# Kernel optimization log

Measured on AMD Instinct MI355X. Metric: run time of the kernel, lower is better.

Reference implementation:

```python
import jax, jax.numpy as jnp
import numpy as np

# DynamicMaskHead config (CondLaneHead defaults, head_layers=3, channels=64)
N, INS_PER_IMG, C, H, W = 4, 8, 64, 160, 256
CIN = C + 2  # coords concatenated
L1, L2, L3 = (C + 2) * C, C * C, C * 1  # weight_nums = [4224, 4096, 64]
B1, B2, B3 = C, C, 1                     # bias_nums   = [64, 64, 1]
NUM_PARAMS = L1 + L2 + L3 + B1 + B2 + B3  # 8513
MASK_BIAS_SHIFT = 2.19  # subtracted from last bias when is_mask=True


def setup_inputs() -> dict:
    key = jax.random.key(0)
    k1, k2 = jax.random.split(key)
    x = jax.random.normal(k1, (N, C, H, W), dtype=jnp.float32)
    mask_head_params = jax.random.normal(k2, (N * INS_PER_IMG, NUM_PARAMS), dtype=jnp.float32) * 0.05
    num_ins = np.full((N,), INS_PER_IMG, dtype=np.int32)  # static per-image instance counts
    return {"x": x, "mask_head_params": mask_head_params, "num_ins": num_ins}


def _locations(h, w, dtype):
    # compute_locations with stride=1: +stride//2 == +0; original normalization
    # (locations[:0], locations[:1]) is a no-op slice, so coords stay unnormalized.
    loc_x = jnp.broadcast_to(jnp.arange(w, dtype=dtype)[None, :], (h, w))
    loc_y = jnp.broadcast_to(jnp.arange(h, dtype=dtype)[:, None], (h, w))
    return jnp.stack([loc_x, loc_y], axis=0)  # [2, H, W]


def reference(x, mask_head_params, num_ins):
    n, _, h, w = x.shape
    loc = _locations(h, w, x.dtype)
    xa = jnp.concatenate([jnp.broadcast_to(loc[None], (n, 2, h, w)), x], axis=1)  # [N, 66, H, W]

    # replicate each image's features per instance (grouped-conv input)
    img_idx = np.repeat(np.arange(n), np.asarray(num_ins))  # static
    num_insts = img_idx.shape[0]
    feats = xa[img_idx].reshape(num_insts, CIN, h * w)  # [I, 66, L]

    # parse_dynamic_params: split flat params into per-instance 1x1 conv weights/biases
    splits = jnp.split(mask_head_params, np.cumsum([L1, L2, L3, B1, B2]), axis=1)
    w0 = splits[0].reshape(num_insts, C, CIN)
    w1 = splits[1].reshape(num_insts, C, C)
    w2 = splits[2].reshape(num_insts, 1, C)
    b0 = splits[3]
    b1 = splits[4]
    b2 = splits[5] - MASK_BIAS_SHIFT  # is_mask=True

    # grouped 1x1 convs == per-instance small matmuls (batched GEMM)
    hdn = jax.nn.relu(jnp.einsum('ioc,icl->iol', w0, feats) + b0[:, :, None])
    hdn = jax.nn.relu(jnp.einsum('ioc,icl->iol', w1, hdn) + b1[:, :, None])
    out = jnp.einsum('ioc,icl->iol', w2, hdn) + b2[:, :, None]  # [I, 1, L]
    return out.reshape(1, num_insts, h, w)
```

## Files before the change

kernel.cpp:

```cpp
#include <hip/hip_runtime.h>
#include <hip/hip_bf16.h>


#define NP 8513
#define HW 40960
#define ISTRIDE 18432
#define OFF_VECA 8192
#define OFF_W1 9216
#define OFF_VECB 17408

typedef __attribute__((ext_vector_type(8))) short bf16x8;
typedef __attribute__((ext_vector_type(4))) float f32x4;
typedef __attribute__((ext_vector_type(2))) unsigned uint2v;

__device__ inline unsigned short f2bf(float f) {
  union { float f; unsigned u; } v; v.f = f;
  unsigned r = v.u + 0x7fffu + ((v.u >> 16) & 1u);
  return (unsigned short)(r >> 16);
}
__device__ inline unsigned pk2(float a, float b) {
  __hip_bfloat162 h = __float22bfloat162_rn(float2{a, b});
  union { __hip_bfloat162 h; unsigned u; } v; v.h = h;
  return v.u;
}
__device__ inline void gld16(const void* g, void* l) {
  __builtin_amdgcn_global_load_lds(
      (const __attribute__((address_space(1))) unsigned*)g,
      (__attribute__((address_space(3))) unsigned*)l, 16, 0, 0);
}

__global__ void condlane_prep(const float* __restrict__ params,
                              char* __restrict__ ws) {
  const int inst = blockIdx.x >> 3, part = blockIdx.x & 7;
  const float* __restrict__ p = params + inst * NP;
  char* base = ws + inst * ISTRIDE;
  const int t = threadIdx.x;
  if (part < 4) {
    unsigned short* dst = (unsigned short*)base;
#pragma unroll
    for (int it = 0; it < 4; it++) {
      const int e = (part * 4 + it) * 256 + t;
      const int frag = e >> 9, lane = (e >> 3) & 63, j = e & 7;
      const int m = (frag >> 1) * 16 + (lane & 15);
      const int k = (frag & 1) * 32 + ((lane >> 4) << 3) + j;
      dst[e] = f2bf(p[m * 66 + 2 + k]);
    }
  } else {
    unsigned short* dst = (unsigned short*)(base + OFF_W1);
#pragma unroll
    for (int it = 0; it < 4; it++) {
      const int e = ((part - 4) * 4 + it) * 256 + t;
      const int frag = e >> 9, lane = (e >> 3) & 63, j = e & 7;
      const int m = (frag >> 1) * 16 + (lane & 15);
      const int k = (frag & 1) * 32 + ((lane >> 4) << 3) + j;
      dst[e] = f2bf(p[4224 + m * 64 + k]);
    }
    if (part == 4) {
      float* vA = (float*)(base + OFF_VECA);
      float* vB = (float*)(base + OFF_VECB);
      if (t < 64) {
        vA[t]       = p[8384 + t];
        vA[64 + t]  = p[t * 66];
        vA[128 + t] = p[t * 66 + 1];
        vB[t]       = p[8448 + t];
        vB[64 + t]  = p[8320 + t];
      } else if (t == 64) vB[128] = p[8512] - 2.19f;
    }
  }
}

__global__ __launch_bounds__(256, 4) void condlane_main(
    const float* __restrict__ x, const char* __restrict__ ws,
    float* __restrict__ out) {
  __shared__ __align__(16) char smem[2 * ISTRIDE];
  const int img = blockIdx.y, bx = blockIdx.x;
  const int tid = threadIdx.x, lane = tid & 63, wave = tid >> 6;
  const int col = lane & 15, q = lane >> 4;
  const char* const wsb = ws + img * 8 * ISTRIDE;

  auto dma = [&](int i, char* buf) {
    const char* src = wsb + i * ISTRIDE;
#pragma unroll
    for (int u = 0; u < 4; u++) {
      const int off = (wave * 4 + u) * 1024;
      gld16(src + off + lane * 16, buf + off);
    }
    if (wave < 2) {
      const int off = (16 + wave) * 1024;
      gld16(src + off + lane * 16, buf + off);
    }
  };
  dma(0, smem);

  bf16x8 bfr[2];
  {
    const float* gx = x + img * 64 * HW + bx * 64 + wave * 16;
#pragma unroll
    for (int ks = 0; ks < 2; ks++) {
      float f[8];
#pragma unroll
      for (int j = 0; j < 8; j++)
        f[j] = gx[(ks * 32 + q * 8 + j) * HW + col];
      union { bf16x8 v; unsigned d[4]; } u;
#pragma unroll
      for (int jj = 0; jj < 4; jj++) u.d[jj] = pk2(f[2 * jj], f[2 * jj + 1]);
      bfr[ks] = u.v;
    }
  }
  __syncthreads();

  const float fyv = (float)(bx >> 2);
  const float fxv = (float)((bx & 3) * 64 + wave * 16 + col);
  float* const outb = out + img * 8 * HW + bx * 64 + wave * 16;

  for (int i = 0; i < 8; i++) {
    char* const wb = smem + (i & 1) * ISTRIDE;
    if (i < 7) dma(i + 1, smem + ((i + 1) & 1) * ISTRIDE);
    const float* const vecA = (const float*)(wb + OFF_VECA);
    const float* const vecB = (const float*)(wb + OFF_VECB);

    f32x4 acc[4];
#pragma unroll
    for (int mt = 0; mt < 4; mt++) {
      const int ro = mt * 16 + q * 4;
      const f32x4 b0v = *(const f32x4*)(vecA + ro);
      const f32x4 wxv = *(const f32x4*)(vecA + 64 + ro);
      const f32x4 wyv = *(const f32x4*)(vecA + 128 + ro);
      acc[mt] = (b0v + wyv * fyv) + wxv * fxv;
    }
#pragma unroll
    for (int mt = 0; mt < 4; mt++) {
      const bf16x8 a0 = *(const bf16x8*)(wb + (mt * 2 + 0) * 1024 + lane * 16);
      const bf16x8 a1 = *(const bf16x8*)(wb + (mt * 2 + 1) * 1024 + lane * 16);
      f32x4 c = __builtin_amdgcn_mfma_f32_16x16x32_bf16(a0, bfr[0], acc[mt], 0, 0, 0);
      acc[mt] = __builtin_amdgcn_mfma_f32_16x16x32_bf16(a1, bfr[1], c, 0, 0, 0);
    }

    unsigned pd[4][2];
#pragma unroll
    for (int mt = 0; mt < 4; mt++) {
      const f32x4 v = acc[mt];
      pd[mt][0] = pk2(fmaxf(v.x, 0.f), fmaxf(v.y, 0.f));
      pd[mt][1] = pk2(fmaxf(v.z, 0.f), fmaxf(v.w, 0.f));
    }
    bf16x8 hbf[2];
#pragma unroll
    for (int ks = 0; ks < 2; ks++) {
      uint2v r0 = __builtin_amdgcn_permlane32_swap(
          pd[2 * ks][0], pd[2 * ks + 1][0], false, false);
      uint2v s0 = __builtin_amdgcn_permlane16_swap(r0[0], r0[1], false, false);
      uint2v r1 = __builtin_amdgcn_permlane32_swap(
          pd[2 * ks][1], pd[2 * ks + 1][1], false, false);
      uint2v s1 = __builtin_amdgcn_permlane16_swap(r1[0], r1[1], false, false);
      union { unsigned d[4]; bf16x8 v; } u;
      u.d[0] = s0[0];
      u.d[1] = s1[0];
      u.d[2] = s0[1];
      u.d[3] = s1[1];
      hbf[ks] = u.v;
    }

    float sA = 0.f, sB = 0.f;
#pragma unroll
    for (int mt = 0; mt < 4; mt++) {
      const bf16x8 a0 = *(const bf16x8*)(wb + OFF_W1 + (mt * 2 + 0) * 1024 + lane * 16);
      const bf16x8 a1 = *(const bf16x8*)(wb + OFF_W1 + (mt * 2 + 1) * 1024 + lane * 16);
      const int ro = mt * 16 + q * 4;
      const f32x4 cb  = *(const f32x4*)(vecB + ro);
      const f32x4 w2v = *(const f32x4*)(vecB + 64 + ro);
      f32x4 c = __builtin_amdgcn_mfma_f32_16x16x32_bf16(a0, hbf[0], cb, 0, 0, 0);
      const f32x4 v = __builtin_amdgcn_mfma_f32_16x16x32_bf16(a1, hbf[1], c, 0, 0, 0);
      float d = w2v.x * fmaxf(v.x, 0.f) + w2v.y * fmaxf(v.y, 0.f) +
                w2v.z * fmaxf(v.z, 0.f) + w2v.w * fmaxf(v.w, 0.f);
      if (mt < 2) sA += d; else sB += d;
    }
    const float b2i = vecB[128];

    float s = sA + sB;
    s += __shfl_xor(s, 16, 64);
    s += __shfl_xor(s, 32, 64);
    if (lane < 16) outb[i * HW + col] = s + b2i;

    if (i < 7) __syncthreads();
  }
}

extern "C" void kernel_launch(void* const* d_in, const int* in_sizes, int n_in,
                              void* d_out, int out_size, void* d_ws, size_t ws_size,
                              hipStream_t stream) {
  const float* x      = (const float*)d_in[0];
  const float* params = (const float*)d_in[1];
  float* out = (float*)d_out;

  condlane_prep<<<256, 256, 0, stream>>>(params, (char*)d_ws);
  condlane_main<<<dim3(640, 4), 256, 0, stream>>>(x, (const char*)d_ws, out);
}
```

Baseline: 124.2 us.

## Process a full 256-pixel row per block to reuse staged weights across 4 tiles

Each block now covers a full image row, 256 pixels, instead of 64, with each wave handling four 16-pixel column tiles. The per-instance weights staged into LDS are reused across four times more MFMA work, cutting LDS staging and sync overhead per pixel. The cost is a larger register footprint (more accumulators and B fragments) and a lower occupancy bound. The grid shrinks to 640 blocks, which may leave CUs underused.

```diff
diff --git a/kernel.cpp b/kernel.cpp
--- a/kernel.cpp
+++ b/kernel.cpp
@@ -69,11 +69,11 @@
   }
 }
 
-__global__ __launch_bounds__(256, 4) void condlane_main(
+__global__ __launch_bounds__(256, 3) void condlane_main(
     const float* __restrict__ x, const char* __restrict__ ws,
     float* __restrict__ out) {
   __shared__ __align__(16) char smem[2 * ISTRIDE];
-  const int img = blockIdx.y, bx = blockIdx.x;
+  const int img = blockIdx.y, row = blockIdx.x;
   const int tid = threadIdx.x, lane = tid & 63, wave = tid >> 6;
   const int col = lane & 15, q = lane >> 4;
   const char* const wsb = ws + img * 8 * ISTRIDE;
@@ -92,26 +92,30 @@
   };
   dma(0, smem);
 
-  bf16x8 bfr[2];
+  bf16x8 bfr[4][2];
   {
-    const float* gx = x + img * 64 * HW + bx * 64 + wave * 16;
-#pragma unroll
-    for (int ks = 0; ks < 2; ks++) {
-      float f[8];
-#pragma unroll
-      for (int j = 0; j < 8; j++)
-        f[j] = gx[(ks * 32 + q * 8 + j) * HW + col];
-      union { bf16x8 v; unsigned d[4]; } u;
-#pragma unroll
-      for (int jj = 0; jj < 4; jj++) u.d[jj] = pk2(f[2 * jj], f[2 * jj + 1]);
-      bfr[ks] = u.v;
-    }
+    const float* gx = x + img * 64 * HW + row * 256 + wave * 64;
+#pragma unroll
+    for (int nt = 0; nt < 4; nt++)
+#pragma unroll
+      for (int ks = 0; ks < 2; ks++) {
+        float f[8];
+#pragma unroll
+        for (int j = 0; j < 8; j++)
+          f[j] = gx[(ks * 32 + q * 8 + j) * HW + nt * 16 + col];
+        union { bf16x8 v; unsigned d[4]; } u;
+#pragma unroll
+        for (int jj = 0; jj < 4; jj++) u.d[jj] = pk2(f[2 * jj], f[2 * jj + 1]);
+        bfr[nt][ks] = u.v;
+      }
   }
   __syncthreads();
 
-  const float fyv = (float)(bx >> 2);
-  const float fxv = (float)((bx & 3) * 64 + wave * 16 + col);
-  float* const outb = out + img * 8 * HW + bx * 64 + wave * 16;
+  const float fyv = (float)row;
+  float fxv[4];
+#pragma unroll
+  for (int nt = 0; nt < 4; nt++) fxv[nt] = (float)(wave * 64 + nt * 16 + col);
+  float* const outb = out + img * 8 * HW + row * 256 + wave * 64;
 
   for (int i = 0; i < 8; i++) {
     char* const wb = smem + (i & 1) * ISTRIDE;
@@ -119,48 +123,58 @@
     const float* const vecA = (const float*)(wb + OFF_VECA);
     const float* const vecB = (const float*)(wb + OFF_VECB);
 
-    f32x4 acc[4];
+    f32x4 acc[4][4];
 #pragma unroll
     for (int mt = 0; mt < 4; mt++) {
       const int ro = mt * 16 + q * 4;
       const f32x4 b0v = *(const f32x4*)(vecA + ro);
       const f32x4 wxv = *(const f32x4*)(vecA + 64 + ro);
       const f32x4 wyv = *(const f32x4*)(vecA + 128 + ro);
-      acc[mt] = (b0v + wyv * fyv) + wxv * fxv;
+      const f32x4 byv = b0v + wyv * fyv;
+#pragma unroll
+      for (int nt = 0; nt < 4; nt++) acc[mt][nt] = byv + wxv * fxv[nt];
     }
 #pragma unroll
     for (int mt = 0; mt < 4; mt++) {
       const bf16x8 a0 = *(const bf16x8*)(wb + (mt * 2 + 0) * 1024 + lane * 16);
       const bf16x8 a1 = *(const bf16x8*)(wb + (mt * 2 + 1) * 1024 + lane * 16);
-      f32x4 c = __builtin_amdgcn_mfma_f32_16x16x32_bf16(a0, bfr[0], acc[mt], 0, 0, 0);
-      acc[mt] = __builtin_amdgcn_mfma_f32_16x16x32_bf16(a1, bfr[1], c, 0, 0, 0);
-    }
-
-    unsigned pd[4][2];
-#pragma unroll
-    for (int mt = 0; mt < 4; mt++) {
-      const f32x4 v = acc[mt];
-      pd[mt][0] = pk2(fmaxf(v.x, 0.f), fmaxf(v.y, 0.f));
-      pd[mt][1] = pk2(fmaxf(v.z, 0.f), fmaxf(v.w, 0.f));
-    }
-    bf16x8 hbf[2];
-#pragma unroll
-    for (int ks = 0; ks < 2; ks++) {
-      uint2v r0 = __builtin_amdgcn_permlane32_swap(
-          pd[2 * ks][0], pd[2 * ks + 1][0], false, false);
-      uint2v s0 = __builtin_amdgcn_permlane16_swap(r0[0], r0[1], false, false);
-      uint2v r1 = __builtin_amdgcn_permlane32_swap(
-          pd[2 * ks][1], pd[2 * ks + 1][1], false, false);
-      uint2v s1 = __builtin_amdgcn_permlane16_swap(r1[0], r1[1], false, false);
-      union { unsigned d[4]; bf16x8 v; } u;
-      u.d[0] = s0[0];
-      u.d[1] = s1[0];
-      u.d[2] = s0[1];
-      u.d[3] = s1[1];
-      hbf[ks] = u.v;
-    }
-
-    float sA = 0.f, sB = 0.f;
+#pragma unroll
+      for (int nt = 0; nt < 4; nt++) {
+        f32x4 c = __builtin_amdgcn_mfma_f32_16x16x32_bf16(a0, bfr[nt][0],
+                                                          acc[mt][nt], 0, 0, 0);
+        acc[mt][nt] = __builtin_amdgcn_mfma_f32_16x16x32_bf16(a1, bfr[nt][1],
+                                                              c, 0, 0, 0);
+      }
+    }
+
+    bf16x8 hbf[4][2];
+#pragma unroll
+    for (int nt = 0; nt < 4; nt++) {
+      unsigned pd[4][2];
+#pragma unroll
+      for (int mt = 0; mt < 4; mt++) {
+        const f32x4 v = acc[mt][nt];
+        pd[mt][0] = pk2(fmaxf(v.x, 0.f), fmaxf(v.y, 0.f));
+        pd[mt][1] = pk2(fmaxf(v.z, 0.f), fmaxf(v.w, 0.f));
+      }
+#pragma unroll
+      for (int ks = 0; ks < 2; ks++) {
+        uint2v r0 = __builtin_amdgcn_permlane32_swap(
+            pd[2 * ks][0], pd[2 * ks + 1][0], false, false);
+        uint2v s0 = __builtin_amdgcn_permlane16_swap(r0[0], r0[1], false, false);
+        uint2v r1 = __builtin_amdgcn_permlane32_swap(
+            pd[2 * ks][1], pd[2 * ks + 1][1], false, false);
+        uint2v s1 = __builtin_amdgcn_permlane16_swap(r1[0], r1[1], false, false);
+        union { unsigned d[4]; bf16x8 v; } u;
+        u.d[0] = s0[0];
+        u.d[1] = s1[0];
+        u.d[2] = s0[1];
+        u.d[3] = s1[1];
+        hbf[nt][ks] = u.v;
+      }
+    }
+
+    float s[4] = {0.f, 0.f, 0.f, 0.f};
 #pragma unroll
     for (int mt = 0; mt < 4; mt++) {
       const bf16x8 a0 = *(const bf16x8*)(wb + OFF_W1 + (mt * 2 + 0) * 1024 + lane * 16);
@@ -168,18 +182,23 @@
       const int ro = mt * 16 + q * 4;
       const f32x4 cb  = *(const f32x4*)(vecB + ro);
       const f32x4 w2v = *(const f32x4*)(vecB + 64 + ro);
-      f32x4 c = __builtin_amdgcn_mfma_f32_16x16x32_bf16(a0, hbf[0], cb, 0, 0, 0);
-      const f32x4 v = __builtin_amdgcn_mfma_f32_16x16x32_bf16(a1, hbf[1], c, 0, 0, 0);
-      float d = w2v.x * fmaxf(v.x, 0.f) + w2v.y * fmaxf(v.y, 0.f) +
-                w2v.z * fmaxf(v.z, 0.f) + w2v.w * fmaxf(v.w, 0.f);
-      if (mt < 2) sA += d; else sB += d;
+#pragma unroll
+      for (int nt = 0; nt < 4; nt++) {
+        f32x4 c = __builtin_amdgcn_mfma_f32_16x16x32_bf16(a0, hbf[nt][0], cb, 0, 0, 0);
+        const f32x4 v = __builtin_amdgcn_mfma_f32_16x16x32_bf16(a1, hbf[nt][1], c, 0, 0, 0);
+        s[nt] += w2v.x * fmaxf(v.x, 0.f) + w2v.y * fmaxf(v.y, 0.f) +
+                 w2v.z * fmaxf(v.z, 0.f) + w2v.w * fmaxf(v.w, 0.f);
+      }
     }
     const float b2i = vecB[128];
 
-    float s = sA + sB;
-    s += __shfl_xor(s, 16, 64);
-    s += __shfl_xor(s, 32, 64);
-    if (lane < 16) outb[i * HW + col] = s + b2i;
+#pragma unroll
+    for (int nt = 0; nt < 4; nt++) {
+      float r = s[nt];
+      r += __shfl_xor(r, 16, 64);
+      r += __shfl_xor(r, 32, 64);
+      if (lane < 16) outb[i * HW + nt * 16 + col] = r + b2i;
+    }
 
     if (i < 7) __syncthreads();
   }
@@ -193,5 +212,5 @@
   float* out = (float*)d_out;
 
   condlane_prep<<<256, 256, 0, stream>>>(params, (char*)d_ws);
-  condlane_main<<<dim3(640, 4), 256, 0, stream>>>(x, (const char*)d_ws, out);
-}
+  condlane_main<<<dim3(160, 4), 256, 0, stream>>>(x, (const char*)d_ws, out);
+}
```

Measured after the change: 122.3 us. About the same (-1.5%).
